# Kernel tuning notes

Hardware: AMD Instinct MI355X
Metric: run time of the kernel (lower is better)

The kernel has to match this reference:

```python
import jax, jax.numpy as jnp
import numpy as np

N_NODES = 50000
N_EDGES = 800000
K = 15          # kernel points
P_DIM = 3
IN_DIM = 32
OUT_DIM = 64
KP_EXTENT = 0.6


def setup_inputs() -> dict:
    key = jax.random.key(0)
    k1, k2, k3, k4, k5, k6 = jax.random.split(key, 6)
    pos = jax.random.normal(k1, (N_NODES, P_DIM), dtype=jnp.float32)
    feat = jax.random.normal(k2, (N_NODES, IN_DIM), dtype=jnp.float32)
    # kernel point layout inside a ball of the given radius (load_kernels stand-in)
    kernel_points = jax.random.normal(k3, (K, P_DIM), dtype=jnp.float32) * 0.5
    kernel_points = kernel_points.at[0].set(0.0)  # fixed center point
    weights = jax.random.normal(k4, (K, IN_DIM, OUT_DIM), dtype=jnp.float32) * (1.0 / np.sqrt(IN_DIM))
    edge_src = jax.random.randint(k5, (N_EDGES,), 0, N_NODES, dtype=jnp.int32)
    edge_dst = jax.random.randint(k6, (N_EDGES,), 0, N_NODES, dtype=jnp.int32)
    return {"pos": pos, "feat": feat, "kernel_points": kernel_points,
            "weights": weights, "edge_src": edge_src, "edge_dst": edge_dst}


def reference(pos, feat, kernel_points, weights, edge_src, edge_dst):
    n_nodes = pos.shape[0]
    # per-edge relative position: src - dst  [E, p]
    y = pos[edge_src] - pos[edge_dst]
    # distance to each kernel point  [E, k]
    diff = y[:, None, :] - kernel_points[None, :, :]
    dist = jnp.sqrt(jnp.sum(diff * diff, axis=-1))
    # linear correlation influence  [E, k]
    m = jax.nn.relu(1.0 - dist / KP_EXTENT)
    # per-edge weighted features  [E, k, in]
    f = feat[edge_src]
    contrib = m[:, :, None] * f[:, None, :]
    # segment-reduce onto destination nodes  [N, k, in]
    weighted_f = jax.ops.segment_sum(contrib, edge_dst, num_segments=n_nodes)
    # per-kernel-point matmul and sum over kernel points  [N, out]
    return jnp.einsum('nki,kio->no', weighted_f, weights)
```

## Files before the change

kernel.cpp:

```cpp
#include <hip/hip_runtime.h>
#include <hip/hip_fp16.h>

#define N_NODES 50000
#define N_EDGES 800000
#define KPTS 15
#define IN_DIM 32
#define OUT_DIM 64
#define KP_EXTENT 0.6f
#define INV_EXT (1.0f / KP_EXTENT)
#define EXT2 (KP_EXTENT * KP_EXTENT)

#define CAP 131072
#define NREP 16
#define SEG_CAP (CAP / NREP)
#define CNT_STRIDE 32
#define K1_BLOCKS (N_EDGES / 256)
#define SUBB 16

#define PCNT_OFF 32768
#define LIST_OFF 262144
#define SLOT_OFF 16777216
#define SCAP_MAX 8

__global__ __launch_bounds__(256) void geom_compact(
    const float* __restrict__ pos,
    const float* __restrict__ kp,
    const int*   __restrict__ esrc,
    const int*   __restrict__ edst,
    int*         __restrict__ cnt,
    int*         __restrict__ pcnt,
    uint2*       __restrict__ lists,
    float4*      __restrict__ outz,
    const int scap)
{
    __shared__ int s_wavecnt[KPTS][4];
    __shared__ int s_woff[KPTS][4];
    __shared__ int s_base[KPTS];

    const int tid  = threadIdx.x;
    const int wv   = tid >> 6;
    const int lane = tid & 63;
    const int rep  = blockIdx.x & (NREP - 1);

    const int e = blockIdx.x * 256 + tid;

    outz[e] = make_float4(0.0f, 0.0f, 0.0f, 0.0f);

    const int s = esrc[e];
    const int d = edst[e];

    const float yx = pos[s * 3 + 0] - pos[d * 3 + 0];
    const float yy = pos[s * 3 + 1] - pos[d * 3 + 1];
    const float yz = pos[s * 3 + 2] - pos[d * 3 + 2];

    float d2v[KPTS];
    unsigned act = 0;
    #pragma unroll
    for (int k = 0; k < KPTS; ++k) {
        const float dx = yx - kp[k * 3 + 0];
        const float dy = yy - kp[k * 3 + 1];
        const float dz = yz - kp[k * 3 + 2];
        const float d2 = dx * dx + dy * dy + dz * dz;
        d2v[k] = d2;
        if (d2 < EXT2) act |= (1u << k);
    }

    #pragma unroll
    for (int k = 0; k < KPTS; ++k) {
        const unsigned long long mask = __ballot((act >> k) & 1u);
        if (lane == 0) s_wavecnt[k][wv] = __popcll(mask);
    }
    __syncthreads();

    if (tid < KPTS) {
        int o0 = 0;
        #pragma unroll
        for (int w = 0; w < 4; ++w) {
            s_woff[tid][w] = o0;
            o0 += s_wavecnt[tid][w];
        }
        s_base[tid] = (o0 > 0)
            ? atomicAdd(&cnt[(tid * NREP + rep) * CNT_STRIDE], o0) : 0;
    }
    __syncthreads();

    const unsigned long long lt = (lane == 63) ? 0x7fffffffffffffffull
                                               : ((1ull << lane) - 1ull);
    #pragma unroll
    for (int k = 0; k < KPTS; ++k) {
        const bool a = (act >> k) & 1u;
        const unsigned long long mask = __ballot(a);
        if (a) {
            const int rank = __popcll(mask & lt);
            const int idx  = s_base[k] + s_woff[k][wv] + rank;
            if (idx < SEG_CAP) {
                const float mk = 1.0f - sqrtf(d2v[k]) * INV_EXT;
                __half hm = __float2half(mk);
                const unsigned mh = *reinterpret_cast<unsigned short*>(&hm);

                const int t = atomicAdd(pcnt + d, 1);
                const unsigned ey = (t < scap)
                    ? (unsigned)((d * scap + t) * OUT_DIM)
                    : (0x80000000u | (unsigned)d);

                lists[(size_t)k * CAP + (size_t)rep * SEG_CAP + idx] =
                    make_uint2(((unsigned)s << 16) | mh, ey);
            }
        }
    }
}

__global__ __launch_bounds__(256) void pair_matmul(
    const float* __restrict__ feat,
    const float* __restrict__ W,
    const int*   __restrict__ cnt,
    const uint2* __restrict__ lists,
    float*       __restrict__ out,
    float*       __restrict__ slots)
{
    const int seg  = blockIdx.x % (KPTS * NREP);
    const int sub  = blockIdx.x / (KPTS * NREP);
    const int k    = seg >> 4;
    const int rep  = seg & (NREP - 1);
    const int wv   = threadIdx.x >> 6;
    const int lane = threadIdx.x & 63;

    float w[IN_DIM];
    #pragma unroll
    for (int i = 0; i < IN_DIM; ++i)
        w[i] = W[k * (IN_DIM * OUT_DIM) + i * OUT_DIM + lane];
    #pragma unroll
    for (int i = 0; i < IN_DIM; ++i)
        asm volatile("" : "+v"(w[i]));

    int n = cnt[seg * CNT_STRIDE];
    if (n > SEG_CAP) n = SEG_CAP;
    const uint2* __restrict__ list =
        lists + (size_t)k * CAP + (size_t)rep * SEG_CAP;

    const int widx    = sub * 4 + wv;
    const int stride2 = SUBB * 4 * 2;

    int base = widx * 2;
    if (base >= n) return;

    uint4 ee = *reinterpret_cast<const uint4*>(list + base);

    for (; base < n; base += stride2) {
        const int nb = base + stride2;
        const uint4 en = *reinterpret_cast<const uint4*>(list + (nb < n ? nb : 0));

        const unsigned ex0 = (unsigned)__builtin_amdgcn_readfirstlane((int)ee.x);
        const unsigned ey0 = (unsigned)__builtin_amdgcn_readfirstlane((int)ee.y);
        const bool two = (base + 1 < n);
        const unsigned ex1 = (unsigned)__builtin_amdgcn_readfirstlane((int)ee.z);
        const unsigned ey1 = (unsigned)__builtin_amdgcn_readfirstlane((int)ee.w);

        __half h0; *reinterpret_cast<unsigned short*>(&h0) = (unsigned short)(ex0 & 0xffffu);
        __half h1; *reinterpret_cast<unsigned short*>(&h1) = (unsigned short)(ex1 & 0xffffu);
        const float m0 = __half2float(h0);
        const float m1 = __half2float(h1);

        const float* __restrict__ f0 = feat + ((ex0 >> 16) << 5);
        const float* __restrict__ f1 = feat + ((ex1 >> 16) << 5);

        if (two) {
            float a0 = 0.0f, b0 = 0.0f, a1 = 0.0f, b1 = 0.0f;
            #pragma unroll
            for (int i = 0; i < 16; ++i) {
                a0 = fmaf(f0[i],      w[i],      a0);
                b0 = fmaf(f0[i + 16], w[i + 16], b0);
                a1 = fmaf(f1[i],      w[i],      a1);
                b1 = fmaf(f1[i + 16], w[i + 16], b1);
            }
            const float r0 = m0 * (a0 + b0);
            const float r1 = m1 * (a1 + b1);

            if (!(ey0 & 0x80000000u)) slots[(size_t)ey0 + lane] = r0;
            else atomicAdd(out + (size_t)(ey0 & 0xffffu) * OUT_DIM + lane, r0);
            if (!(ey1 & 0x80000000u)) slots[(size_t)ey1 + lane] = r1;
            else atomicAdd(out + (size_t)(ey1 & 0xffffu) * OUT_DIM + lane, r1);
        } else {
            float a0 = 0.0f, b0 = 0.0f;
            #pragma unroll
            for (int i = 0; i < 16; ++i) {
                a0 = fmaf(f0[i],      w[i],      a0);
                b0 = fmaf(f0[i + 16], w[i + 16], b0);
            }
            const float r0 = m0 * (a0 + b0);
            if (!(ey0 & 0x80000000u)) slots[(size_t)ey0 + lane] = r0;
            else atomicAdd(out + (size_t)(ey0 & 0xffffu) * OUT_DIM + lane, r0);
        }

        ee = en;
    }
}

__global__ __launch_bounds__(256) void node_reduce(
    const int*   __restrict__ pcnt,
    const float* __restrict__ slots,
    float*       __restrict__ out,
    const int scap)
{
    const int wv   = threadIdx.x >> 6;
    const int lane = threadIdx.x & 63;
    const int node = blockIdx.x * 4 + wv;

    const int raw = pcnt[node];
    int deg = raw;
    if (deg > scap) deg = scap;

    const float* __restrict__ sp = slots + ((size_t)node * scap) * OUT_DIM + lane;

    float a0 = (raw > scap) ? out[(size_t)node * OUT_DIM + lane] : 0.0f;
    float a1 = 0.0f;

    int j = 0;
    for (; j + 1 < deg; j += 2) {
        a0 += sp[(size_t)j * OUT_DIM];
        a1 += sp[(size_t)(j + 1) * OUT_DIM];
    }
    if (j < deg) a1 += sp[(size_t)j * OUT_DIM];

    out[(size_t)node * OUT_DIM + lane] = a0 + a1;
}

extern "C" void kernel_launch(void* const* d_in, const int* in_sizes, int n_in,
                              void* d_out, int out_size, void* d_ws, size_t ws_size,
                              hipStream_t stream)
{
    const float* pos  = (const float*)d_in[0];
    const float* feat = (const float*)d_in[1];
    const float* kp   = (const float*)d_in[2];
    const float* W    = (const float*)d_in[3];
    const int* esrc   = (const int*)d_in[4];
    const int* edst   = (const int*)d_in[5];
    float* out        = (float*)d_out;

    int*   cnt   = (int*)d_ws;
    int*   pcnt  = (int*)((char*)d_ws + PCNT_OFF);
    uint2* lists = (uint2*)((char*)d_ws + LIST_OFF);
    float* slots = (float*)((char*)d_ws + SLOT_OFF);

    const size_t layer_bytes = (size_t)N_NODES * OUT_DIM * sizeof(float);
    int scap = 0;
    if (ws_size >= (size_t)SLOT_OFF + layer_bytes) {
        scap = (int)((ws_size - (size_t)SLOT_OFF) / layer_bytes);
        if (scap > SCAP_MAX) scap = SCAP_MAX;
    }

    hipMemsetAsync(d_ws, 0, LIST_OFF, stream);

    geom_compact<<<K1_BLOCKS, 256, 0, stream>>>(pos, kp, esrc, edst, cnt, pcnt,
                                                lists, (float4*)out, scap);
    pair_matmul<<<SUBB * KPTS * NREP, 256, 0, stream>>>(feat, W, cnt, lists,
                                                        out, slots);
    if (scap > 0)
        node_reduce<<<N_NODES / 4, 256, 0, stream>>>(pcnt, slots, out, scap);
}
```

Before: 134.2 us.

## Use fp16 features, weights and slots with fdot2 and software-pipelined gathers

Converts node features to packed fp16 inside the geometry kernel, packs the weights to fp16 and computes each per-pair dot product with fdot2. Partial results are stored as fp16 pairs in per-node slots, which halves slot traffic; the slot cap is raised to 16 and the reduce kernel reads packed halves. The feature gather is prefetched one iteration ahead to hide latency. In exchange it gives up precision (fp16 products and partial sums) and adds more register pressure.

```diff
diff --git a/kernel.cpp b/kernel.cpp
--- a/kernel.cpp
+++ b/kernel.cpp
@@ -18,18 +18,48 @@
 #define SUBB 16
 
 #define PCNT_OFF 32768
-#define LIST_OFF 262144
-#define SLOT_OFF 16777216
-#define SCAP_MAX 8
+#define FEATH_OFF (1u << 20)
+#define LIST_OFF  (8u << 20)
+#define SLOT_OFF  (32u << 20)
+#define SCAP_MAX 16
+
+typedef unsigned int uint;
+
+#define RFL(x) ((uint)__builtin_amdgcn_readfirstlane((int)(x)))
+
+static __device__ __forceinline__ float h2f16(uint u) {
+    return __half2float(__ushort_as_half((unsigned short)(u & 0xffffu)));
+}
+static __device__ __forceinline__ uint pack2(float lo, float hi) {
+    return (uint)__half_as_ushort(__float2half_rn(lo))
+         | ((uint)__half_as_ushort(__float2half_rn(hi)) << 16);
+}
+
+#if __has_builtin(__builtin_amdgcn_fdot2)
+typedef _Float16 h2v __attribute__((ext_vector_type(2)));
+static __device__ __forceinline__ float fdot2u(uint a, uint b, float c) {
+    union U { uint u; h2v h; };
+    U ua, ub; ua.u = a; ub.u = b;
+    return __builtin_amdgcn_fdot2(ua.h, ub.h, c, false);
+}
+#else
+static __device__ __forceinline__ float fdot2u(uint a, uint b, float c) {
+    const float al = h2f16(a), ah = h2f16(a >> 16);
+    const float bl = h2f16(b), bh = h2f16(b >> 16);
+    return fmaf(ah, bh, fmaf(al, bl, c));
+}
+#endif
 
 __global__ __launch_bounds__(256) void geom_compact(
     const float* __restrict__ pos,
+    const float* __restrict__ feat,
     const float* __restrict__ kp,
     const int*   __restrict__ esrc,
     const int*   __restrict__ edst,
     int*         __restrict__ cnt,
     int*         __restrict__ pcnt,
     uint2*       __restrict__ lists,
+    uint*        __restrict__ featH,
     float4*      __restrict__ outz,
     const int scap)
 {
@@ -45,6 +75,10 @@
     const int e = blockIdx.x * 256 + tid;
 
     outz[e] = make_float4(0.0f, 0.0f, 0.0f, 0.0f);
+    {
+        const float2 fv = ((const float2*)feat)[e];
+        featH[e] = pack2(fv.x, fv.y);
+    }
 
     const int s = esrc[e];
     const int d = edst[e];
@@ -96,7 +130,7 @@
             if (idx < SEG_CAP) {
                 const float mk = 1.0f - sqrtf(d2v[k]) * INV_EXT;
                 __half hm = __float2half(mk);
-                const unsigned mh = *reinterpret_cast<unsigned short*>(&hm);
+                const unsigned mh = (unsigned)__half_as_ushort(hm);
 
                 const int t = atomicAdd(pcnt + d, 1);
                 const unsigned ey = (t < scap)
@@ -111,12 +145,12 @@
 }
 
 __global__ __launch_bounds__(256) void pair_matmul(
-    const float* __restrict__ feat,
+    const uint*  __restrict__ featH,
     const float* __restrict__ W,
     const int*   __restrict__ cnt,
     const uint2* __restrict__ lists,
     float*       __restrict__ out,
-    float*       __restrict__ slots)
+    uint*        __restrict__ slots16)
 {
     const int seg  = blockIdx.x % (KPTS * NREP);
     const int sub  = blockIdx.x / (KPTS * NREP);
@@ -125,13 +159,16 @@
     const int wv   = threadIdx.x >> 6;
     const int lane = threadIdx.x & 63;
 
-    float w[IN_DIM];
-    #pragma unroll
-    for (int i = 0; i < IN_DIM; ++i)
-        w[i] = W[k * (IN_DIM * OUT_DIM) + i * OUT_DIM + lane];
-    #pragma unroll
-    for (int i = 0; i < IN_DIM; ++i)
-        asm volatile("" : "+v"(w[i]));
+    uint wpk[16];
+    #pragma unroll
+    for (int j = 0; j < 16; ++j) {
+        const float wa = W[k * (IN_DIM * OUT_DIM) + (2 * j)     * OUT_DIM + lane];
+        const float wb = W[k * (IN_DIM * OUT_DIM) + (2 * j + 1) * OUT_DIM + lane];
+        wpk[j] = pack2(wa, wb);
+    }
+    #pragma unroll
+    for (int j = 0; j < 16; ++j)
+        asm volatile("" : "+v"(wpk[j]));
 
     int n = cnt[seg * CNT_STRIDE];
     if (n > SEG_CAP) n = SEG_CAP;
@@ -144,85 +181,114 @@
     int base = widx * 2;
     if (base >= n) return;
 
-    uint4 ee = *reinterpret_cast<const uint4*>(list + base);
+    uint4 eeA = *reinterpret_cast<const uint4*>(list + base);
+    const int bB0 = base + stride2;
+    uint4 eeB = *reinterpret_cast<const uint4*>(list + (bB0 < n ? bB0 : 0));
+
+    uint axA0 = RFL(eeA.x), ayA0 = RFL(eeA.y),
+         axA1 = RFL(eeA.z), ayA1 = RFL(eeA.w);
+    uint sA0 = axA0 >> 16; if (sA0 >= N_NODES) sA0 = 0;
+    uint sA1 = axA1 >> 16; if (sA1 >= N_NODES) sA1 = 0;
+    uint faA[16], fbA[16];
+    {
+        const uint* __restrict__ p0 = featH + sA0 * 16;
+        const uint* __restrict__ p1 = featH + sA1 * 16;
+        #pragma unroll
+        for (int j = 0; j < 16; ++j) { faA[j] = p0[j]; fbA[j] = p1[j]; }
+    }
 
     for (; base < n; base += stride2) {
-        const int nb = base + stride2;
-        const uint4 en = *reinterpret_cast<const uint4*>(list + (nb < n ? nb : 0));
-
-        const unsigned ex0 = (unsigned)__builtin_amdgcn_readfirstlane((int)ee.x);
-        const unsigned ey0 = (unsigned)__builtin_amdgcn_readfirstlane((int)ee.y);
-        const bool two = (base + 1 < n);
-        const unsigned ex1 = (unsigned)__builtin_amdgcn_readfirstlane((int)ee.z);
-        const unsigned ey1 = (unsigned)__builtin_amdgcn_readfirstlane((int)ee.w);
-
-        __half h0; *reinterpret_cast<unsigned short*>(&h0) = (unsigned short)(ex0 & 0xffffu);
-        __half h1; *reinterpret_cast<unsigned short*>(&h1) = (unsigned short)(ex1 & 0xffffu);
-        const float m0 = __half2float(h0);
-        const float m1 = __half2float(h1);
-
-        const float* __restrict__ f0 = feat + ((ex0 >> 16) << 5);
-        const float* __restrict__ f1 = feat + ((ex1 >> 16) << 5);
-
+        const int bC = base + 2 * stride2;
+        const uint4 eeC = *reinterpret_cast<const uint4*>(list + (bC < n ? bC : 0));
+
+        const uint axB0 = RFL(eeB.x), ayB0 = RFL(eeB.y),
+                   axB1 = RFL(eeB.z), ayB1 = RFL(eeB.w);
+        uint sB0 = axB0 >> 16; if (sB0 >= N_NODES) sB0 = 0;
+        uint sB1 = axB1 >> 16; if (sB1 >= N_NODES) sB1 = 0;
+        uint faB[16], fbB[16];
+        {
+            const uint* __restrict__ p0 = featH + sB0 * 16;
+            const uint* __restrict__ p1 = featH + sB1 * 16;
+            #pragma unroll
+            for (int j = 0; j < 16; ++j) { faB[j] = p0[j]; fbB[j] = p1[j]; }
+        }
+
+        float acc0 = 0.0f, acc1 = 0.0f;
+        #pragma unroll
+        for (int j = 0; j < 16; ++j) {
+            acc0 = fdot2u(faA[j], wpk[j], acc0);
+            acc1 = fdot2u(fbA[j], wpk[j], acc1);
+        }
+        const float m0 = h2f16(axA0);
+        const float m1 = h2f16(axA1);
+        const float r0 = m0 * acc0;
+        const float r1 = m1 * acc1;
+        const bool  two = (base + 1 < n);
+
+        const float p0 = __shfl_xor(r0, 1);
+        const float p1 = __shfl_xor(r1, 1);
+
+        if (!(ayA0 & 0x80000000u)) {
+            if (!(lane & 1))
+                slots16[(ayA0 >> 1) + (lane >> 1)] = pack2(r0, p0);
+        } else {
+            atomicAdd(out + (size_t)(ayA0 & 0xffffu) * OUT_DIM + lane, r0);
+        }
         if (two) {
-            float a0 = 0.0f, b0 = 0.0f, a1 = 0.0f, b1 = 0.0f;
-            #pragma unroll
-            for (int i = 0; i < 16; ++i) {
-                a0 = fmaf(f0[i],      w[i],      a0);
-                b0 = fmaf(f0[i + 16], w[i + 16], b0);
-                a1 = fmaf(f1[i],      w[i],      a1);
-                b1 = fmaf(f1[i + 16], w[i + 16], b1);
+            if (!(ayA1 & 0x80000000u)) {
+                if (!(lane & 1))
+                    slots16[(ayA1 >> 1) + (lane >> 1)] = pack2(r1, p1);
+            } else {
+                atomicAdd(out + (size_t)(ayA1 & 0xffffu) * OUT_DIM + lane, r1);
             }
-            const float r0 = m0 * (a0 + b0);
-            const float r1 = m1 * (a1 + b1);
-
-            if (!(ey0 & 0x80000000u)) slots[(size_t)ey0 + lane] = r0;
-            else atomicAdd(out + (size_t)(ey0 & 0xffffu) * OUT_DIM + lane, r0);
-            if (!(ey1 & 0x80000000u)) slots[(size_t)ey1 + lane] = r1;
-            else atomicAdd(out + (size_t)(ey1 & 0xffffu) * OUT_DIM + lane, r1);
-        } else {
-            float a0 = 0.0f, b0 = 0.0f;
-            #pragma unroll
-            for (int i = 0; i < 16; ++i) {
-                a0 = fmaf(f0[i],      w[i],      a0);
-                b0 = fmaf(f0[i + 16], w[i + 16], b0);
-            }
-            const float r0 = m0 * (a0 + b0);
-            if (!(ey0 & 0x80000000u)) slots[(size_t)ey0 + lane] = r0;
-            else atomicAdd(out + (size_t)(ey0 & 0xffffu) * OUT_DIM + lane, r0);
-        }
-
-        ee = en;
+        }
+
+        axA0 = axB0; ayA0 = ayB0; axA1 = axB1; ayA1 = ayB1;
+        #pragma unroll
+        for (int j = 0; j < 16; ++j) { faA[j] = faB[j]; fbA[j] = fbB[j]; }
+        eeB = eeC;
     }
 }
 
 __global__ __launch_bounds__(256) void node_reduce(
-    const int*   __restrict__ pcnt,
-    const float* __restrict__ slots,
-    float*       __restrict__ out,
+    const int*  __restrict__ pcnt,
+    const uint* __restrict__ slots16,
+    float*      __restrict__ out,
     const int scap)
 {
     const int wv   = threadIdx.x >> 6;
     const int lane = threadIdx.x & 63;
     const int node = blockIdx.x * 4 + wv;
 
+    if (lane >= 32) return;
+
     const int raw = pcnt[node];
     int deg = raw;
     if (deg > scap) deg = scap;
 
-    const float* __restrict__ sp = slots + ((size_t)node * scap) * OUT_DIM + lane;
-
-    float a0 = (raw > scap) ? out[(size_t)node * OUT_DIM + lane] : 0.0f;
-    float a1 = 0.0f;
-
+    const uint* __restrict__ sp =
+        slots16 + (size_t)node * ((size_t)scap * 32) + lane;
+
+    float a0 = 0.0f, a1 = 0.0f, b0 = 0.0f, b1 = 0.0f;
     int j = 0;
     for (; j + 1 < deg; j += 2) {
-        a0 += sp[(size_t)j * OUT_DIM];
-        a1 += sp[(size_t)(j + 1) * OUT_DIM];
-    }
-    if (j < deg) a1 += sp[(size_t)j * OUT_DIM];
-
-    out[(size_t)node * OUT_DIM + lane] = a0 + a1;
+        const uint u0 = sp[(size_t)j * 32];
+        const uint u1 = sp[(size_t)(j + 1) * 32];
+        a0 += h2f16(u0); a1 += h2f16(u0 >> 16);
+        b0 += h2f16(u1); b1 += h2f16(u1 >> 16);
+    }
+    if (j < deg) {
+        const uint u0 = sp[(size_t)j * 32];
+        a0 += h2f16(u0); a1 += h2f16(u0 >> 16);
+    }
+
+    float o0 = a0 + b0;
+    float o1 = a1 + b1;
+    if (raw > scap) {
+        const float2 prev = ((const float2*)out)[(size_t)node * 32 + lane];
+        o0 += prev.x; o1 += prev.y;
+    }
+    ((float2*)out)[(size_t)node * 32 + lane] = make_float2(o0, o1);
 }
 
 extern "C" void kernel_launch(void* const* d_in, const int* in_sizes, int n_in,
@@ -237,24 +303,26 @@
     const int* edst   = (const int*)d_in[5];
     float* out        = (float*)d_out;
 
-    int*   cnt   = (int*)d_ws;
-    int*   pcnt  = (int*)((char*)d_ws + PCNT_OFF);
-    uint2* lists = (uint2*)((char*)d_ws + LIST_OFF);
-    float* slots = (float*)((char*)d_ws + SLOT_OFF);
-
-    const size_t layer_bytes = (size_t)N_NODES * OUT_DIM * sizeof(float);
+    int*   cnt     = (int*)d_ws;
+    int*   pcnt    = (int*)((char*)d_ws + PCNT_OFF);
+    uint*  featH   = (uint*)((char*)d_ws + FEATH_OFF);
+    uint2* lists   = (uint2*)((char*)d_ws + LIST_OFF);
+    uint*  slots16 = (uint*)((char*)d_ws + SLOT_OFF);
+
+    const size_t layer_bytes = (size_t)N_NODES * OUT_DIM * 2;
     int scap = 0;
     if (ws_size >= (size_t)SLOT_OFF + layer_bytes) {
         scap = (int)((ws_size - (size_t)SLOT_OFF) / layer_bytes);
         if (scap > SCAP_MAX) scap = SCAP_MAX;
     }
 
-    hipMemsetAsync(d_ws, 0, LIST_OFF, stream);
-
-    geom_compact<<<K1_BLOCKS, 256, 0, stream>>>(pos, kp, esrc, edst, cnt, pcnt,
-                                                lists, (float4*)out, scap);
-    pair_matmul<<<SUBB * KPTS * NREP, 256, 0, stream>>>(feat, W, cnt, lists,
-                                                        out, slots);
+    hipMemsetAsync(d_ws, 0, 262144, stream);
+
+    geom_compact<<<K1_BLOCKS, 256, 0, stream>>>(pos, feat, kp, esrc, edst,
+                                                cnt, pcnt, lists, featH,
+                                                (float4*)out, scap);
+    pair_matmul<<<SUBB * KPTS * NREP, 256, 0, stream>>>(featH, W, cnt, lists,
+                                                        out, slots16);
     if (scap > 0)
-        node_reduce<<<N_NODES / 4, 256, 0, stream>>>(pcnt, slots, out, scap);
-}
+        node_reduce<<<N_NODES / 4, 256, 0, stream>>>(pcnt, slots16, out, scap);
+}
```

After: 134.2 us. Within noise of the previous version (-0.0%).
